# Kernel optimization log

Hardware: AMD Instinct MI355X
Metric: run time of the kernel (lower is better)

Reference implementation:

```python
import jax, jax.numpy as jnp
import numpy as np

DIM = 1024
NUM_HEADS = 16
HEAD_DIM = DIM // NUM_HEADS


def _rope_tables(seq_len, dim, dtype):
    # matches llama_rotary_embedding: inv_freq over even indices of head_dim
    inv_freq = 1.0 / (10000.0 ** (jnp.arange(0, dim, 2, dtype=jnp.float32) / dim))
    t = jnp.arange(seq_len, dtype=jnp.float32)
    freqs = jnp.outer(t, inv_freq)  # [S, dim/2]
    return jnp.cos(freqs).astype(dtype), jnp.sin(freqs).astype(dtype)


def _apply_rope(x, cos_emb, sin_emb):
    # x: [B, H, S, hd]; takes interleaved halves, concatenates rotated halves
    x1 = x[..., 0::2]
    x2 = x[..., 1::2]
    return jnp.concatenate((x1 * cos_emb - x2 * sin_emb,
                            x1 * sin_emb + x2 * cos_emb), axis=-1)


def setup_inputs() -> dict:
    key = jax.random.key(0)
    k_x, k_qkv, k_out, k_b = jax.random.split(key, 4)
    B, S, D = 2, 2048, DIM
    x = jax.random.normal(k_x, (B, S, D), dtype=jnp.float32)
    # torch nn.Linear weights are [out_features, in_features]
    w_qkv = jax.random.normal(k_qkv, (3 * D, D), dtype=jnp.float32) * (1.0 / np.sqrt(D))
    w_out = jax.random.normal(k_out, (D, D), dtype=jnp.float32) * (1.0 / np.sqrt(D))
    b_out = jax.random.normal(k_b, (D,), dtype=jnp.float32) * 0.01
    return {"x": x, "w_qkv": w_qkv, "w_out": w_out, "b_out": b_out}


def reference(x, w_qkv, w_out, b_out):
    B, S, D = x.shape
    H, hd = NUM_HEADS, HEAD_DIM
    qkv = jnp.einsum('bsd,ed->bse', x, w_qkv)  # [B, S, 3D]
    q, k, v = jnp.split(qkv, 3, axis=-1)
    # [B, S, D] -> [B, H, S, hd]
    q, k, v = (t.reshape(B, S, H, hd).transpose(0, 2, 1, 3) for t in (q, k, v))
    cos_emb, sin_emb = _rope_tables(S, hd, x.dtype)  # [S, hd/2]
    q = _apply_rope(q, cos_emb, sin_emb)
    k = _apply_rope(k, cos_emb, sin_emb)
    scores = jnp.einsum('bhqd,bhkd->bhqk', q, k) / jnp.sqrt(jnp.asarray(hd, x.dtype))
    attn = jax.nn.softmax(scores, axis=-1)
    out = jnp.einsum('bhqk,bhkd->bhqd', attn, v)
    out = out.transpose(0, 2, 1, 3).reshape(B, S, D)
    return jnp.einsum('bsd,ed->bse', out, w_out) + b_out
```

## Files before the change

kernel.cpp:

```cpp
#include <hip/hip_runtime.h>
#include <math.h>

typedef __bf16 bf16_t;
typedef bf16_t bf16x8 __attribute__((ext_vector_type(8)));
typedef bf16_t bf16x4 __attribute__((ext_vector_type(4)));
typedef short  s16x4  __attribute__((ext_vector_type(4)));
typedef float  f32x4  __attribute__((ext_vector_type(4)));

#define DIM_   1024
#define NHEADS 16
#define HDIM   64
#define SEQ    2048
#define BATCH  2

#define QK_SCALE 0.18033688011112042f

__device__ __forceinline__ s16x4 as_s16x4(bf16x4 v) {
    union { bf16x4 b; s16x4 s; } u; u.b = v; return u.s;
}

__device__ __forceinline__ void gld16(const bf16_t* g, bf16_t* l) {
    __builtin_amdgcn_global_load_lds(
        (const __attribute__((address_space(1))) void*)g,
        (__attribute__((address_space(3))) void*)l, 16, 0, 0);
}

#define XCNT   (4096u * 1024u)
#define WQCNT  (3072u * 1024u)
#define WOCNT  (1024u * 1024u)
__global__ __launch_bounds__(256) void cast3(const float* __restrict__ s0,
                                             const float* __restrict__ s1,
                                             const float* __restrict__ s2,
                                             bf16_t* __restrict__ d0,
                                             bf16_t* __restrict__ d1,
                                             bf16_t* __restrict__ d2) {
    size_t i = ((size_t)blockIdx.x * 256 + threadIdx.x) * 8;
    const float* s; bf16_t* d; size_t off;
    if (i < XCNT)               { s = s0; d = d0; off = i; }
    else if (i < XCNT + WQCNT)  { s = s1; d = d1; off = i - XCNT; }
    else                        { s = s2; d = d2; off = i - XCNT - WQCNT; }
    float4 a = *(const float4*)(s + off);
    float4 b = *(const float4*)(s + off + 4);
    bf16x8 o = { (bf16_t)a.x, (bf16_t)a.y, (bf16_t)a.z, (bf16_t)a.w,
                 (bf16_t)b.x, (bf16_t)b.y, (bf16_t)b.z, (bf16_t)b.w };
    *(bf16x8*)(d + off) = o;
}

template <bool QKV>
__global__ __launch_bounds__(256) void gemm_lds(const bf16_t* __restrict__ A,
                                                const bf16_t* __restrict__ B,
                                                const float* __restrict__ bias,
                                                void* __restrict__ Cout,
                                                bf16_t* __restrict__ vt,
                                                int M, int N, int K) {
    __shared__ __align__(16) bf16_t As[128 * 32];
    __shared__ __align__(16) bf16_t Bs[128 * 32];
    const int tid  = threadIdx.x;
    const int m0   = blockIdx.y * 128;
    const int n0   = blockIdx.x * 128;
    const int w    = tid >> 6;
    const int lane = tid & 63;
    const int m16  = lane & 15;
    const int quad = lane >> 4;
    const int wm   = (w >> 1) * 64;
    const int wn   = (w & 1) * 64;
    const int lrow = lane >> 2;
    const int lcol = (lane & 3) * 8;

    const bf16_t* pa0 = A + (size_t)(m0 + w * 16 + lrow) * K + lcol;
    const bf16_t* pb0 = B + (size_t)(n0 + w * 16 + lrow) * K + lcol;
    bf16_t* lA0 = &As[(w * 16) * 32];
    bf16_t* lA1 = &As[(64 + w * 16) * 32];
    bf16_t* lB0 = &Bs[(w * 16) * 32];
    bf16_t* lB1 = &Bs[(64 + w * 16) * 32];

    f32x4 acc[4][4] = {};

    for (int k0 = 0; k0 < K; k0 += 32) {
        __syncthreads();
        gld16(pa0 + k0, lA0);
        gld16(pa0 + (size_t)64 * K + k0, lA1);
        gld16(pb0 + k0, lB0);
        gld16(pb0 + (size_t)64 * K + k0, lB1);
        __syncthreads();

        bf16x8 af[4], bfr[4];
#pragma unroll
        for (int i = 0; i < 4; ++i)
            af[i] = *(const bf16x8*)(&As[(wm + i * 16 + m16) * 32 + quad * 8]);
#pragma unroll
        for (int j = 0; j < 4; ++j)
            bfr[j] = *(const bf16x8*)(&Bs[(wn + j * 16 + m16) * 32 + quad * 8]);
#pragma unroll
        for (int i = 0; i < 4; ++i)
#pragma unroll
            for (int j = 0; j < 4; ++j)
                acc[i][j] = __builtin_amdgcn_mfma_f32_16x16x32_bf16(af[i], bfr[j], acc[i][j], 0, 0, 0);
    }

    if (QKV && n0 >= 2 * DIM_) {
        const int b      = m0 >> 11;
        const int s_base = (m0 & (SEQ - 1)) + wm;
#pragma unroll
        for (int j = 0; j < 4; ++j) {
            const int cit = wn + j * 16 + m16;
            const int h   = ((n0 - 2 * DIM_) >> 6) + (cit >> 6);
            const int d   = cit & 63;
            bf16_t* vrow = vt + ((size_t)(b * 16 + h) * 64 + d) * SEQ + s_base;
#pragma unroll
            for (int i = 0; i < 4; ++i) {
                bf16x4 ov = { (bf16_t)acc[i][j][0], (bf16_t)acc[i][j][1],
                              (bf16_t)acc[i][j][2], (bf16_t)acc[i][j][3] };
                *(bf16x4*)(vrow + i * 16 + quad * 4) = ov;
            }
        }
    } else if (QKV) {
        bf16_t* C = (bf16_t*)Cout;
#pragma unroll
        for (int i = 0; i < 4; ++i)
#pragma unroll
            for (int j = 0; j < 4; ++j) {
                const int col = n0 + wn + j * 16 + m16;
#pragma unroll
                for (int r = 0; r < 4; ++r)
                    C[(size_t)(m0 + wm + i * 16 + quad * 4 + r) * N + col] = (bf16_t)acc[i][j][r];
            }
    } else {
        float* C = (float*)Cout;
#pragma unroll
        for (int j = 0; j < 4; ++j) {
            const int col = n0 + wn + j * 16 + m16;
            const float bv = bias[col];
#pragma unroll
            for (int i = 0; i < 4; ++i)
#pragma unroll
                for (int r = 0; r < 4; ++r)
                    C[(size_t)(m0 + wm + i * 16 + quad * 4 + r) * N + col] = acc[i][j][r] + bv;
        }
    }
}

__global__ __launch_bounds__(256) void rope_bf16(bf16_t* __restrict__ qkv) {
    __shared__ float ctab[8][32];
    __shared__ float stab[8][32];
    const int tid = threadIdx.x;
    const int sl  = tid >> 5, j = tid & 31;
    const int s   = (int)((blockIdx.x * 8 + sl) & (SEQ - 1));
    const float freq = exp2f(-0.41524101186092029f * (float)j);
    float sn, cs;
    sincosf((float)s * freq, &sn, &cs);
    ctab[sl][j] = cs;
    stab[sl][j] = sn;
    __syncthreads();

    const int gid   = blockIdx.x * 256 + tid;
    const int m     = gid >> 5;
    const int rr    = gid & 31;
    const int which = rr >> 4;
    const int hh    = rr & 15;
    const float osc = (which == 0) ? QK_SCALE : 1.0f;

    bf16_t* p = qkv + (size_t)m * (3 * DIM_) + which * DIM_ + hh * HDIM;
    union { bf16_t e[64]; bf16x8 v[8]; } X, O;
#pragma unroll
    for (int i = 0; i < 8; ++i) X.v[i] = *(const bf16x8*)(p + i * 8);
#pragma unroll
    for (int t = 0; t < 32; ++t) {
        const float x1 = (float)X.e[2 * t];
        const float x2 = (float)X.e[2 * t + 1];
        const float c  = ctab[sl][t];
        const float s2 = stab[sl][t];
        O.e[t]      = (bf16_t)((x1 * c - x2 * s2) * osc);
        O.e[32 + t] = (bf16_t)((x1 * s2 + x2 * c) * osc);
    }
#pragma unroll
    for (int i = 0; i < 8; ++i) *(bf16x8*)(p + i * 8) = O.v[i];
}

__global__ __launch_bounds__(256) void attn_mfma(const bf16_t* __restrict__ qkv,
                                                 const bf16_t* __restrict__ vt,
                                                 bf16_t* __restrict__ out) {
    __shared__ __align__(16) char smem[18432];
    bf16_t* Ks   = (bf16_t*)smem;
    bf16_t* Vt   = (bf16_t*)(smem + 9216);
    float*  Ored = (float*)smem;
    float*  Lred = (float*)(smem + 16640);

    const int tid  = threadIdx.x;
    const int w    = tid >> 6;
    const int lane = tid & 63;
    const int m16  = lane & 15;
    const int quad = lane >> 4;
    const int bh   = blockIdx.y;
    const int b    = bh >> 4;
    const int hh   = bh & 15;
    const int q0   = blockIdx.x * 64;

    const size_t rs = 3 * DIM_;
    const bf16_t* qbase = qkv + (size_t)(b * SEQ) * rs + hh * HDIM;
    const bf16_t* kbase = qbase + DIM_;
    const bf16_t* vtg   = vt + (size_t)bh * 64 * SEQ;

    bf16x8 qf[4][2];
#pragma unroll
    for (int n = 0; n < 4; ++n)
#pragma unroll
        for (int kt = 0; kt < 2; ++kt)
            qf[n][kt] = *(const bf16x8*)(qbase + (size_t)(q0 + n * 16 + m16) * rs + kt * 32 + quad * 8);

    f32x4 o[4][4] = {};
    float lp[4] = {};

    const int srow = tid >> 3;
    const int sc8  = (tid & 7) * 8;

    bf16x8 kreg[2], vreg[2];
#pragma unroll
    for (int p = 0; p < 2; ++p) {
        const int row = srow + p * 32;
        kreg[p] = *(const bf16x8*)(kbase + (size_t)row * rs + sc8);
        vreg[p] = *(const bf16x8*)(vtg + (size_t)row * SEQ + sc8);
    }

    for (int t = 0; t < 32; ++t) {
        __syncthreads();
#pragma unroll
        for (int p = 0; p < 2; ++p) {
            const int row = srow + p * 32;
            *(bf16x8*)(&Ks[row * 72 + sc8]) = kreg[p];
            *(bf16x8*)(&Vt[row * 72 + sc8]) = vreg[p];
        }
        __syncthreads();

        if (t < 31) {
            const size_t k0n = (size_t)(t + 1) * 64;
#pragma unroll
            for (int p = 0; p < 2; ++p) {
                const int row = srow + p * 32;
                kreg[p] = *(const bf16x8*)(kbase + (k0n + row) * rs + sc8);
                vreg[p] = *(const bf16x8*)(vtg + (size_t)row * SEQ + k0n + sc8);
            }
        }

        bf16x8 ak0 = *(const bf16x8*)(&Ks[(w * 16 + m16) * 72 + 0 * 32 + quad * 8]);
        bf16x8 ak1 = *(const bf16x8*)(&Ks[(w * 16 + m16) * 72 + 1 * 32 + quad * 8]);
        bf16x4 va[4];
#pragma unroll
        for (int ds = 0; ds < 4; ++ds)
            va[ds] = *(const bf16x4*)(&Vt[(ds * 16 + m16) * 72 + w * 16 + quad * 4]);

        s16x4 pb[4];
#pragma unroll
        for (int n = 0; n < 4; ++n) {
            f32x4 c = {};
            c = __builtin_amdgcn_mfma_f32_16x16x32_bf16(ak0, qf[n][0], c, 0, 0, 0);
            c = __builtin_amdgcn_mfma_f32_16x16x32_bf16(ak1, qf[n][1], c, 0, 0, 0);
            bf16x4 pv;
#pragma unroll
            for (int r = 0; r < 4; ++r) {
                const float p = __builtin_amdgcn_exp2f(c[r]);
                lp[n] += p;
                pv[r] = (bf16_t)p;
            }
            pb[n] = as_s16x4(pv);
        }

#pragma unroll
        for (int ds = 0; ds < 4; ++ds)
#pragma unroll
            for (int n = 0; n < 4; ++n)
                o[ds][n] = __builtin_amdgcn_mfma_f32_16x16x16bf16_1k(as_s16x4(va[ds]), pb[n], o[ds][n], 0, 0, 0);
    }

#pragma unroll
    for (int n = 0; n < 4; ++n) {
        lp[n] += __shfl_xor(lp[n], 16);
        lp[n] += __shfl_xor(lp[n], 32);
    }
    __syncthreads();
    if (quad == 0) {
#pragma unroll
        for (int n = 0; n < 4; ++n) Lred[w * 64 + n * 16 + m16] = lp[n];
    }
    __syncthreads();
    const float linv = 1.0f / (Lred[lane] + Lred[64 + lane] + Lred[128 + lane] + Lred[192 + lane]);

    const size_t obase = (size_t)(b * SEQ + q0 + lane) * DIM_ + hh * HDIM;
#pragma unroll
    for (int p = 0; p < 4; ++p) {
        __syncthreads();
#pragma unroll
        for (int n = 0; n < 4; ++n)
#pragma unroll
            for (int r = 0; r < 4; ++r)
                Ored[w * 1040 + (quad * 4 + r) * 65 + n * 16 + m16] = o[p][n][r];
        __syncthreads();
        if (w == p) {
            union { bf16_t e[16]; bf16x8 v[2]; } ob;
#pragma unroll
            for (int d = 0; d < 16; ++d) {
                const float v = Ored[d * 65 + lane] + Ored[1040 + d * 65 + lane] +
                                Ored[2080 + d * 65 + lane] + Ored[3120 + d * 65 + lane];
                ob.e[d] = (bf16_t)(v * linv);
            }
            *(bf16x8*)(out + obase + p * 16)     = ob.v[0];
            *(bf16x8*)(out + obase + p * 16 + 8) = ob.v[1];
        }
    }
}

extern "C" void kernel_launch(void* const* d_in, const int* in_sizes, int n_in,
                              void* d_out, int out_size, void* d_ws, size_t ws_size,
                              hipStream_t stream) {
    const float* x     = (const float*)d_in[0];
    const float* w_qkv = (const float*)d_in[1];
    const float* w_out = (const float*)d_in[2];
    const float* b_out = (const float*)d_in[3];
    float* out = (float*)d_out;

    const int M = BATCH * SEQ;

    bf16_t* qkv_b  = (bf16_t*)d_ws;
    bf16_t* attn_b = qkv_b + (size_t)M * 3 * DIM_;
    bf16_t* vt_b   = attn_b + (size_t)M * DIM_;
    bf16_t* xb     = vt_b + (size_t)BATCH * NHEADS * HDIM * SEQ;
    bf16_t* wqkvb  = xb + (size_t)M * DIM_;
    bf16_t* woutb  = wqkvb + (size_t)3 * DIM_ * DIM_;

    cast3<<<(XCNT + WQCNT + WOCNT) / (256 * 8), 256, 0, stream>>>(
        x, w_qkv, w_out, xb, wqkvb, woutb);

    gemm_lds<true><<<dim3(3 * DIM_ / 128, M / 128), 256, 0, stream>>>(
        xb, wqkvb, nullptr, qkv_b, vt_b, M, 3 * DIM_, DIM_);

    rope_bf16<<<(M * 2 * NHEADS) / 256, 256, 0, stream>>>(qkv_b);

    attn_mfma<<<dim3(SEQ / 64, BATCH * NHEADS), 256, 0, stream>>>(qkv_b, vt_b, attn_b);

    gemm_lds<false><<<dim3(DIM_ / 128, M / 128), 256, 0, stream>>>(
        attn_b, woutb, b_out, out, nullptr, M, DIM_, DIM_);
}
```

Measured before the change: 226.5 us.

## Load K/V MFMA fragments directly from global memory instead of staging through LDS

The attention loop no longer stages each 64-key K and V^T tile through shared memory with two barriers per iteration. Each wave now reads its own MFMA operand fragments straight from global memory, and the pointers advance by one tile per step. This removes the LDS round trip, the register double-buffer and the per-iteration __syncthreads, and raises wave priority around the PV MFMA block. In exchange the global loads are no longer prefetched a tile ahead, so their latency is exposed, and the access pattern is narrower per row, relying on cache reuse across the block. The smem size shrinks, and a barrier before the Lred write is dropped, which is safe only because the loop no longer uses LDS.

```diff
diff --git a/kernel.cpp b/kernel.cpp
--- a/kernel.cpp
+++ b/kernel.cpp
@@ -180,11 +180,9 @@
 __global__ __launch_bounds__(256) void attn_mfma(const bf16_t* __restrict__ qkv,
                                                  const bf16_t* __restrict__ vt,
                                                  bf16_t* __restrict__ out) {
-    __shared__ __align__(16) char smem[18432];
-    bf16_t* Ks   = (bf16_t*)smem;
-    bf16_t* Vt   = (bf16_t*)(smem + 9216);
-    float*  Ored = (float*)smem;
-    float*  Lred = (float*)(smem + 16640);
+    __shared__ __align__(16) char smem[17664];
+    float* Ored = (float*)smem;
+    float* Lred = (float*)(smem + 16640);
 
     const int tid  = threadIdx.x;
     const int w    = tid >> 6;
@@ -211,43 +209,16 @@
     f32x4 o[4][4] = {};
     float lp[4] = {};
 
-    const int srow = tid >> 3;
-    const int sc8  = (tid & 7) * 8;
-
-    bf16x8 kreg[2], vreg[2];
-#pragma unroll
-    for (int p = 0; p < 2; ++p) {
-        const int row = srow + p * 32;
-        kreg[p] = *(const bf16x8*)(kbase + (size_t)row * rs + sc8);
-        vreg[p] = *(const bf16x8*)(vtg + (size_t)row * SEQ + sc8);
-    }
+    const bf16_t* kp = kbase + (size_t)(w * 16 + m16) * rs + quad * 8;
+    const bf16_t* vp = vtg + (size_t)m16 * SEQ + w * 16 + quad * 4;
 
     for (int t = 0; t < 32; ++t) {
-        __syncthreads();
-#pragma unroll
-        for (int p = 0; p < 2; ++p) {
-            const int row = srow + p * 32;
-            *(bf16x8*)(&Ks[row * 72 + sc8]) = kreg[p];
-            *(bf16x8*)(&Vt[row * 72 + sc8]) = vreg[p];
-        }
-        __syncthreads();
-
-        if (t < 31) {
-            const size_t k0n = (size_t)(t + 1) * 64;
-#pragma unroll
-            for (int p = 0; p < 2; ++p) {
-                const int row = srow + p * 32;
-                kreg[p] = *(const bf16x8*)(kbase + (k0n + row) * rs + sc8);
-                vreg[p] = *(const bf16x8*)(vtg + (size_t)row * SEQ + k0n + sc8);
-            }
-        }
-
-        bf16x8 ak0 = *(const bf16x8*)(&Ks[(w * 16 + m16) * 72 + 0 * 32 + quad * 8]);
-        bf16x8 ak1 = *(const bf16x8*)(&Ks[(w * 16 + m16) * 72 + 1 * 32 + quad * 8]);
+        bf16x8 ak0 = *(const bf16x8*)(kp);
+        bf16x8 ak1 = *(const bf16x8*)(kp + 32);
         bf16x4 va[4];
 #pragma unroll
         for (int ds = 0; ds < 4; ++ds)
-            va[ds] = *(const bf16x4*)(&Vt[(ds * 16 + m16) * 72 + w * 16 + quad * 4]);
+            va[ds] = *(const bf16x4*)(vp + (size_t)ds * 16 * SEQ);
 
         s16x4 pb[4];
 #pragma unroll
@@ -265,11 +236,16 @@
             pb[n] = as_s16x4(pv);
         }
 
+        __builtin_amdgcn_s_setprio(1);
 #pragma unroll
         for (int ds = 0; ds < 4; ++ds)
 #pragma unroll
             for (int n = 0; n < 4; ++n)
                 o[ds][n] = __builtin_amdgcn_mfma_f32_16x16x16bf16_1k(as_s16x4(va[ds]), pb[n], o[ds][n], 0, 0, 0);
+        __builtin_amdgcn_s_setprio(0);
+
+        kp += (size_t)64 * rs;
+        vp += 64;
     }
 
 #pragma unroll
@@ -277,7 +253,6 @@
         lp[n] += __shfl_xor(lp[n], 16);
         lp[n] += __shfl_xor(lp[n], 32);
     }
-    __syncthreads();
     if (quad == 0) {
 #pragma unroll
         for (int n = 0; n < 4; ++n) Lred[w * 64 + n * 16 + m16] = lp[n];
```

Result: slower. 250.9 us (+10.8%).
